# Performance work log

Measured on AMD Instinct MI355X. Metric: run time of the kernel, lower is better.

Reference implementation:

```python
import jax, jax.numpy as jnp
import numpy as np

STATE_DIM, ACTION_DIM, HIDDEN_DIM, GRU_DIM = 256, 64, 1024, 512
BATCH = 65536
IN_DIM = STATE_DIM + ACTION_DIM


def setup_inputs() -> dict:
    key = jax.random.key(0)
    ks = jax.random.split(key, 12)
    s = lambda k, shp, scale: (jax.random.normal(k, shp, jnp.float32) * scale)
    inp = {
        'state': jax.random.normal(ks[0], (BATCH, STATE_DIM), jnp.float32),
        'action': jax.random.normal(ks[1], (BATCH, ACTION_DIM), jnp.float32),
        'hidden': jax.random.normal(ks[2], (1, BATCH, GRU_DIM), jnp.float32),
        # GRU params, PyTorch layout: rows ordered [reset, update, new]
        'w_ih': s(ks[3], (3 * GRU_DIM, IN_DIM), 0.05),
        'w_hh': s(ks[4], (3 * GRU_DIM, GRU_DIM), 0.05),
        'b_ih': jnp.zeros((3 * GRU_DIM,), jnp.float32),
        'b_hh': jnp.zeros((3 * GRU_DIM,), jnp.float32),
        'w1': s(ks[5], (HIDDEN_DIM, GRU_DIM), 0.05),
        'b1': jnp.zeros((HIDDEN_DIM,), jnp.float32),
        'w2': s(ks[6], (HIDDEN_DIM, HIDDEN_DIM), 0.03),
        'b2': jnp.zeros((HIDDEN_DIM,), jnp.float32),
        'w3': s(ks[7], (1, HIDDEN_DIM), 0.03),
        'b3': jnp.zeros((1,), jnp.float32),
    }
    return inp


def reference(state, action, hidden, w_ih, w_hh, b_ih, b_hh, w1, b1, w2, b2, w3, b3):
    # (state, action) -> concat -> single-step GRU -> fc1 -> relu -> fc2 -> relu -> fc3
    sa = jnp.concatenate([state, action], axis=1)          # [B, IN_DIM]
    h = hidden[0]                                           # [B, G]
    gi = sa @ w_ih.T + b_ih                                 # [B, 3G]
    gh = h @ w_hh.T + b_hh                                  # [B, 3G]
    G = h.shape[1]
    i_r, i_z, i_n = gi[:, :G], gi[:, G:2 * G], gi[:, 2 * G:]
    h_r, h_z, h_n = gh[:, :G], gh[:, G:2 * G], gh[:, 2 * G:]
    r = jax.nn.sigmoid(i_r + h_r)
    z = jax.nn.sigmoid(i_z + h_z)
    n = jnp.tanh(i_n + r * h_n)
    h_new = (1.0 - z) * n + z * h                           # [B, G]
    x = jax.nn.relu(h_new @ w1.T + b1)
    x = jax.nn.relu(x @ w2.T + b2)
    q = x @ w3.T + b3                                       # [B, 1]
    return q, h_new[None]
```

## Files before the change

kernel.cpp:

```cpp
#include <hip/hip_runtime.h>
#include <stdint.h>

#define BATCH 65536
#define KCAT 832

typedef __attribute__((ext_vector_type(8))) short bf16x8;
typedef __attribute__((ext_vector_type(4))) float f32x4;

typedef __attribute__((address_space(3))) void lds_void_t;
typedef __attribute__((address_space(1))) void glob_void_t;

__device__ __forceinline__ void async_copy16(const void* g, void* l) {
  __builtin_amdgcn_global_load_lds((glob_void_t*)(uintptr_t)g,
                                   (lds_void_t*)(uint32_t)(uintptr_t)l, 16, 0, 0);
}

__device__ __forceinline__ float b2f(unsigned short u) {
  union { uint32_t i; float f; } c; c.i = ((uint32_t)u) << 16; return c.f;
}
__device__ __forceinline__ unsigned short f2b(float f) {
  uint32_t x = __float_as_uint(f);
  uint32_t r = (x + 0x7fffu + ((x >> 16) & 1u)) >> 16;
  return (unsigned short)r;
}


__global__ void pack_A(const float* __restrict__ state, const float* __restrict__ action,
                       const float* __restrict__ hidden, unsigned short* __restrict__ Acat) {
  long t = (long)blockIdx.x * 256 + threadIdx.x;
  int seg = (int)(t % 104); long row = t / 104;
  int col = seg * 8;
  const float* src;
  if (col < 256)       src = state  + row * 256 + col;
  else if (col < 320)  src = action + row * 64  + (col - 256);
  else                 src = hidden + row * 512 + (col - 320);
  bf16x8 o;
  #pragma unroll
  for (int j = 0; j < 8; j++) o[j] = (short)f2b(src[j]);
  *(bf16x8*)(Acat + row * (size_t)KCAT + col) = o;
}

__global__ void pack_W(const float* __restrict__ w_ih, const float* __restrict__ w_hh,
                       unsigned short* __restrict__ Wrz, unsigned short* __restrict__ Wn) {
  long t = (long)blockIdx.x * 256 + threadIdx.x;
  int seg = (int)(t % 104); int j = (int)(t / 104);
  int col = seg * 8;
  const float* src = (col < 320) ? (w_ih + (long)j * 320 + col)
                                 : (w_hh + (long)j * 512 + (col - 320));
  unsigned short* dst = (j < 1024) ? (Wrz + (long)j * KCAT + col)
                                   : (Wn + (long)(j - 1024) * KCAT + col);
  bf16x8 o;
  #pragma unroll
  for (int jj = 0; jj < 8; jj++) o[jj] = (short)f2b(src[jj]);
  *(bf16x8*)dst = o;
}

__global__ void pack_w12(const float* __restrict__ w1, const float* __restrict__ w2,
                         unsigned short* __restrict__ w1b, unsigned short* __restrict__ w2b) {
  long t = (long)blockIdx.x * 256 + threadIdx.x;
  const float* s; unsigned short* d;
  if (t < 65536) { s = w1 + t * 8; d = w1b + t * 8; }
  else           { long t2 = t - 65536; s = w2 + t2 * 8; d = w2b + t2 * 8; }
  bf16x8 o;
  #pragma unroll
  for (int j = 0; j < 8; j++) o[j] = (short)f2b(s[j]);
  *(bf16x8*)d = o;
}


__global__ __launch_bounds__(256, 2) void gru_fused(
    const unsigned short* __restrict__ A,
    const unsigned short* __restrict__ Wrz,
    const unsigned short* __restrict__ Wn,
    const float* __restrict__ b_ih, const float* __restrict__ b_hh,
    float* __restrict__ hnew_f,
    unsigned short* __restrict__ hnew_b)
{
  __shared__ unsigned short Asm[128 * 64];
  __shared__ unsigned short Wsm[3 * 64 * 64];
  const int tid = threadIdx.x;
  const int wave = tid >> 6, lane = tid & 63;
  const int wm = wave >> 1, wn = wave & 1;

  const int bid = blockIdx.x;
  const int xcd = bid & 7;
  const int j = bid >> 3;
  const int bn = j & 7;
  const long bm = (long)xcd * 64 + (j >> 3);

  const int srow = lane >> 3;
  const int scol = (lane & 7) * 8;

  f32x4 accR[4][2], accZ[4][2], accI[4][2], accH[4][2];
  #pragma unroll
  for (int i = 0; i < 4; i++)
    #pragma unroll
    for (int t = 0; t < 2; t++) {
      accR[i][t] = (f32x4){0.f,0.f,0.f,0.f}; accZ[i][t] = (f32x4){0.f,0.f,0.f,0.f};
      accI[i][t] = (f32x4){0.f,0.f,0.f,0.f}; accH[i][t] = (f32x4){0.f,0.f,0.f,0.f};
    }

  const unsigned short* Ag  = A   + (bm * 128 + wave * 8 + srow) * (size_t)KCAT + scol;
  const unsigned short* Wrg = Wrz + ((size_t)bn * 64 + wave * 8 + srow) * KCAT + scol;
  const unsigned short* Wzg = Wrz + ((size_t)512 + bn * 64 + wave * 8 + srow) * KCAT + scol;
  const unsigned short* Wng = Wn  + ((size_t)bn * 64 + wave * 8 + srow) * KCAT + scol;

  for (int kt = 0; kt < 13; ++kt) {
    __syncthreads();
    #pragma unroll
    for (int t = 0; t < 4; ++t)
      async_copy16(Ag + (size_t)(t * 32) * KCAT + kt * 64, &Asm[(t * 32 + wave * 8) * 64]);
    #pragma unroll
    for (int t = 0; t < 2; ++t) {
      async_copy16(Wrg + (size_t)(t * 32) * KCAT + kt * 64, &Wsm[0 * 4096 + (t * 32 + wave * 8) * 64]);
      async_copy16(Wzg + (size_t)(t * 32) * KCAT + kt * 64, &Wsm[1 * 4096 + (t * 32 + wave * 8) * 64]);
      async_copy16(Wng + (size_t)(t * 32) * KCAT + kt * 64, &Wsm[2 * 4096 + (t * 32 + wave * 8) * 64]);
    }
    __syncthreads();

    #pragma unroll
    for (int ks = 0; ks < 2; ++ks) {
      const int kcol = ks * 32 + (lane >> 4) * 8;
      bf16x8 af[4], bR[2], bZ[2], bN[2];
      #pragma unroll
      for (int mt = 0; mt < 4; mt++)
        af[mt] = *(const bf16x8*)&Asm[(wm * 64 + mt * 16 + (lane & 15)) * 64 + kcol];
      #pragma unroll
      for (int nt = 0; nt < 2; nt++) {
        const int wrow = (wn * 32 + nt * 16 + (lane & 15)) * 64 + kcol;
        bR[nt] = *(const bf16x8*)&Wsm[0 * 4096 + wrow];
        bZ[nt] = *(const bf16x8*)&Wsm[1 * 4096 + wrow];
        bN[nt] = *(const bf16x8*)&Wsm[2 * 4096 + wrow];
      }
      #pragma unroll
      for (int mt = 0; mt < 4; mt++)
        #pragma unroll
        for (int nt = 0; nt < 2; nt++) {
          accR[mt][nt] = __builtin_amdgcn_mfma_f32_16x16x32_bf16(af[mt], bR[nt], accR[mt][nt], 0, 0, 0);
          accZ[mt][nt] = __builtin_amdgcn_mfma_f32_16x16x32_bf16(af[mt], bZ[nt], accZ[mt][nt], 0, 0, 0);
        }
      if (kt < 5) {
        #pragma unroll
        for (int mt = 0; mt < 4; mt++)
          #pragma unroll
          for (int nt = 0; nt < 2; nt++)
            accI[mt][nt] = __builtin_amdgcn_mfma_f32_16x16x32_bf16(af[mt], bN[nt], accI[mt][nt], 0, 0, 0);
      } else {
        #pragma unroll
        for (int mt = 0; mt < 4; mt++)
          #pragma unroll
          for (int nt = 0; nt < 2; nt++)
            accH[mt][nt] = __builtin_amdgcn_mfma_f32_16x16x32_bf16(af[mt], bN[nt], accH[mt][nt], 0, 0, 0);
      }
    }
  }

  const long rowbase = bm * 128 + wm * 64;
  const int colbase = bn * 64 + wn * 32;
  #pragma unroll
  for (int mt = 0; mt < 4; mt++) {
    #pragma unroll
    for (int nt = 0; nt < 2; nt++) {
      const int col = colbase + nt * 16 + (lane & 15);
      const float brv = b_ih[col] + b_hh[col];
      const float bzv = b_ih[512 + col] + b_hh[512 + col];
      const float bin = b_ih[1024 + col];
      const float bhn = b_hh[1024 + col];
      #pragma unroll
      for (int i = 0; i < 4; i++) {
        const long row = rowbase + mt * 16 + (lane >> 4) * 4 + i;
        const float r = 1.f / (1.f + __expf(-(accR[mt][nt][i] + brv)));
        const float z = 1.f / (1.f + __expf(-(accZ[mt][nt][i] + bzv)));
        const float x = (accI[mt][nt][i] + bin) + r * (accH[mt][nt][i] + bhn);
        const float n = 1.f - 2.f / (__expf(2.f * x) + 1.f);
        const float h = b2f(A[row * (size_t)KCAT + 320 + col]);
        const float hv = (1.f - z) * n + z * h;
        hnew_f[row * (size_t)512 + col] = hv;
        hnew_b[row * (size_t)512 + col] = f2b(hv);
      }
    }
  }
}


template<int KT>
__global__ __launch_bounds__(256, 2) void gemm_bt(
    const unsigned short* __restrict__ A, const unsigned short* __restrict__ W,
    const float* __restrict__ bias, unsigned short* __restrict__ out,
    int lda)
{
  __shared__ unsigned short Asm[128 * 64];
  __shared__ unsigned short Bsm[128 * 64];
  const int tid = threadIdx.x;
  const int wave = tid >> 6, lane = tid & 63;
  const int wm = wave >> 1, wn = wave & 1;

  const int bid = blockIdx.x;
  const int xcd = bid & 7;
  const int j = bid >> 3;
  const int bn = j & 7;
  const long bm = (long)xcd * 64 + (j >> 3);

  const int srow = lane >> 3;
  const int scol = (lane & 7) * 8;

  f32x4 acc[4][4];
  #pragma unroll
  for (int i = 0; i < 4; i++)
    #pragma unroll
    for (int t = 0; t < 4; t++) acc[i][t] = (f32x4){0.f, 0.f, 0.f, 0.f};

  const unsigned short* Ag = A + (bm * 128 + wave * 8 + srow) * (size_t)lda + scol;
  const unsigned short* Wg = W + ((size_t)bn * 128 + wave * 8 + srow) * lda + scol;

  for (int kt = 0; kt < KT; ++kt) {
    __syncthreads();
    #pragma unroll
    for (int t = 0; t < 4; ++t)
      async_copy16(Ag + (size_t)(t * 32) * lda + kt * 64, &Asm[(t * 32 + wave * 8) * 64]);
    #pragma unroll
    for (int t = 0; t < 4; ++t)
      async_copy16(Wg + (size_t)(t * 32) * lda + kt * 64, &Bsm[(t * 32 + wave * 8) * 64]);
    __syncthreads();

    #pragma unroll
    for (int ks = 0; ks < 2; ++ks) {
      const int kcol = ks * 32 + (lane >> 4) * 8;
      bf16x8 af[4], bfv[4];
      #pragma unroll
      for (int mt = 0; mt < 4; mt++)
        af[mt] = *(const bf16x8*)&Asm[(wm * 64 + mt * 16 + (lane & 15)) * 64 + kcol];
      #pragma unroll
      for (int nt = 0; nt < 4; nt++)
        bfv[nt] = *(const bf16x8*)&Bsm[(wn * 64 + nt * 16 + (lane & 15)) * 64 + kcol];
      #pragma unroll
      for (int mt = 0; mt < 4; mt++)
        #pragma unroll
        for (int nt = 0; nt < 4; nt++)
          acc[mt][nt] = __builtin_amdgcn_mfma_f32_16x16x32_bf16(af[mt], bfv[nt], acc[mt][nt], 0, 0, 0);
    }
  }

  #pragma unroll
  for (int mt = 0; mt < 4; mt++) {
    #pragma unroll
    for (int nt = 0; nt < 4; nt++) {
      const int col = bn * 128 + wn * 64 + nt * 16 + (lane & 15);
      const float bv = bias[col];
      #pragma unroll
      for (int i = 0; i < 4; i++) {
        const long row = bm * 128 + wm * 64 + mt * 16 + (lane >> 4) * 4 + i;
        float v = fmaxf(acc[mt][nt][i] + bv, 0.f);
        out[row * (size_t)1024 + col] = f2b(v);
      }
    }
  }
}


__global__ void qdot(const unsigned short* __restrict__ x2, const float* __restrict__ w3,
                     const float* __restrict__ b3, float* __restrict__ q) {
  const int lane = threadIdx.x & 63;
  const long row = (long)blockIdx.x * 4 + (threadIdx.x >> 6);
  const unsigned short* xr = x2 + row * (size_t)1024 + lane * 8;
  bf16x8 v0 = *(const bf16x8*)xr;
  bf16x8 v1 = *(const bf16x8*)(xr + 512);
  float s = 0.f;
  #pragma unroll
  for (int j = 0; j < 8; j++) {
    s += b2f((unsigned short)v0[j]) * w3[lane * 8 + j];
    s += b2f((unsigned short)v1[j]) * w3[512 + lane * 8 + j];
  }
  #pragma unroll
  for (int off = 32; off > 0; off >>= 1) s += __shfl_down(s, off, 64);
  if (lane == 0) q[row] = s + b3[0];
}


extern "C" void kernel_launch(void* const* d_in, const int* in_sizes, int n_in,
                              void* d_out, int out_size, void* d_ws, size_t ws_size,
                              hipStream_t stream) {
  const float* state  = (const float*)d_in[0];
  const float* action = (const float*)d_in[1];
  const float* hidden = (const float*)d_in[2];
  const float* w_ih   = (const float*)d_in[3];
  const float* w_hh   = (const float*)d_in[4];
  const float* b_ih   = (const float*)d_in[5];
  const float* b_hh   = (const float*)d_in[6];
  const float* w1     = (const float*)d_in[7];
  const float* b1     = (const float*)d_in[8];
  const float* w2     = (const float*)d_in[9];
  const float* b2     = (const float*)d_in[10];
  const float* w3     = (const float*)d_in[11];
  const float* b3     = (const float*)d_in[12];

  float* q_out = (float*)d_out;
  float* h_out = q_out + BATCH;

  char* ws = (char*)d_ws;
  unsigned short* Acat = (unsigned short*)(ws + 0);
  unsigned short* x1   = (unsigned short*)(ws + 0);
  unsigned short* x2   = (unsigned short*)(ws + 134217728);
  unsigned short* hnb  = (unsigned short*)(ws + 268435456);
  unsigned short* Wrz  = (unsigned short*)(ws + 335544320);
  unsigned short* Wn   = (unsigned short*)(ws + 337248256);
  unsigned short* w1b  = (unsigned short*)(ws + 338100224);
  unsigned short* w2b  = (unsigned short*)(ws + 339148800);

  pack_A<<<26624, 256, 0, stream>>>(state, action, hidden, Acat);
  pack_W<<<624, 256, 0, stream>>>(w_ih, w_hh, Wrz, Wn);
  pack_w12<<<768, 256, 0, stream>>>(w1, w2, w1b, w2b);

  gru_fused<<<4096, 256, 0, stream>>>(Acat, Wrz, Wn, b_ih, b_hh, h_out, hnb);
  gemm_bt<8><<<4096, 256, 0, stream>>>(hnb, w1b, b1, x1, 512);
  gemm_bt<16><<<4096, 256, 0, stream>>>(x1, w2b, b2, x2, 1024);
  qdot<<<16384, 256, 0, stream>>>(x2, w3, b3, q_out);
}
```

Baseline: 821.4 us.

## Swizzle LDS tiles and fuse fc3 dot product into fc2 GEMM epilogue

Applies an XOR swizzle to the LDS column layout in both the GRU and generic GEMM kernels, so MFMA fragment reads avoid bank conflicts. Fuses the final fc3 reduction into the fc2 GEMM epilogue: each block computes partial dot products with w3, reduces them across lanes and atomically adds into q, which is pre-initialized with b3 in the weight pack kernel. This removes the 128MB x2 write/read and the separate qdot launch. In exchange it adds float atomics, whose summation order is nondeterministic.

```diff
diff --git a/kernel.cpp b/kernel.cpp
--- a/kernel.cpp
+++ b/kernel.cpp
@@ -56,15 +56,26 @@
 }
 
 __global__ void pack_w12(const float* __restrict__ w1, const float* __restrict__ w2,
-                         unsigned short* __restrict__ w1b, unsigned short* __restrict__ w2b) {
+                         const float* __restrict__ b3,
+                         unsigned short* __restrict__ w1b, unsigned short* __restrict__ w2b,
+                         float* __restrict__ q) {
   long t = (long)blockIdx.x * 256 + threadIdx.x;
-  const float* s; unsigned short* d;
-  if (t < 65536) { s = w1 + t * 8; d = w1b + t * 8; }
-  else           { long t2 = t - 65536; s = w2 + t2 * 8; d = w2b + t2 * 8; }
-  bf16x8 o;
-  #pragma unroll
-  for (int j = 0; j < 8; j++) o[j] = (short)f2b(s[j]);
-  *(bf16x8*)d = o;
+  if (t < 65536) {
+    const float* s = w1 + t * 8; unsigned short* d = w1b + t * 8;
+    bf16x8 o;
+    #pragma unroll
+    for (int j = 0; j < 8; j++) o[j] = (short)f2b(s[j]);
+    *(bf16x8*)d = o;
+  } else if (t < 196608) {
+    long t2 = t - 65536;
+    const float* s = w2 + t2 * 8; unsigned short* d = w2b + t2 * 8;
+    bf16x8 o;
+    #pragma unroll
+    for (int j = 0; j < 8; j++) o[j] = (short)f2b(s[j]);
+    *(bf16x8*)d = o;
+  } else {
+    q[t - 196608] = b3[0];
+  }
 }
 
 
@@ -89,7 +100,7 @@
   const long bm = (long)xcd * 64 + (j >> 3);
 
   const int srow = lane >> 3;
-  const int scol = (lane & 7) * 8;
+  const int scol = (((lane & 7) ^ srow)) * 8;
 
   f32x4 accR[4][2], accZ[4][2], accI[4][2], accH[4][2];
   #pragma unroll
@@ -105,6 +116,9 @@
   const unsigned short* Wzg = Wrz + ((size_t)512 + bn * 64 + wave * 8 + srow) * KCAT + scol;
   const unsigned short* Wng = Wn  + ((size_t)bn * 64 + wave * 8 + srow) * KCAT + scol;
 
+  const int rlo = lane & 15;
+  const int quad = lane >> 4;
+
   for (int kt = 0; kt < 13; ++kt) {
     __syncthreads();
     #pragma unroll
@@ -120,14 +134,15 @@
 
     #pragma unroll
     for (int ks = 0; ks < 2; ++ks) {
-      const int kcol = ks * 32 + (lane >> 4) * 8;
+      const int kseg = ks * 4 + quad;
+      const int sw = (kseg ^ (rlo & 7)) * 8;
       bf16x8 af[4], bR[2], bZ[2], bN[2];
       #pragma unroll
       for (int mt = 0; mt < 4; mt++)
-        af[mt] = *(const bf16x8*)&Asm[(wm * 64 + mt * 16 + (lane & 15)) * 64 + kcol];
+        af[mt] = *(const bf16x8*)&Asm[(wm * 64 + mt * 16 + rlo) * 64 + sw];
       #pragma unroll
       for (int nt = 0; nt < 2; nt++) {
-        const int wrow = (wn * 32 + nt * 16 + (lane & 15)) * 64 + kcol;
+        const int wrow = (wn * 32 + nt * 16 + rlo) * 64 + sw;
         bR[nt] = *(const bf16x8*)&Wsm[0 * 4096 + wrow];
         bZ[nt] = *(const bf16x8*)&Wsm[1 * 4096 + wrow];
         bN[nt] = *(const bf16x8*)&Wsm[2 * 4096 + wrow];
@@ -161,14 +176,14 @@
   for (int mt = 0; mt < 4; mt++) {
     #pragma unroll
     for (int nt = 0; nt < 2; nt++) {
-      const int col = colbase + nt * 16 + (lane & 15);
+      const int col = colbase + nt * 16 + rlo;
       const float brv = b_ih[col] + b_hh[col];
       const float bzv = b_ih[512 + col] + b_hh[512 + col];
       const float bin = b_ih[1024 + col];
       const float bhn = b_hh[1024 + col];
       #pragma unroll
       for (int i = 0; i < 4; i++) {
-        const long row = rowbase + mt * 16 + (lane >> 4) * 4 + i;
+        const long row = rowbase + mt * 16 + quad * 4 + i;
         const float r = 1.f / (1.f + __expf(-(accR[mt][nt][i] + brv)));
         const float z = 1.f / (1.f + __expf(-(accZ[mt][nt][i] + bzv)));
         const float x = (accI[mt][nt][i] + bin) + r * (accH[mt][nt][i] + bhn);
@@ -183,11 +198,11 @@
 }
 
 
-template<int KT>
+template<int KT, int QFUSE>
 __global__ __launch_bounds__(256, 2) void gemm_bt(
     const unsigned short* __restrict__ A, const unsigned short* __restrict__ W,
     const float* __restrict__ bias, unsigned short* __restrict__ out,
-    int lda)
+    int lda, const float* __restrict__ w3, float* __restrict__ q)
 {
   __shared__ unsigned short Asm[128 * 64];
   __shared__ unsigned short Bsm[128 * 64];
@@ -202,7 +217,7 @@
   const long bm = (long)xcd * 64 + (j >> 3);
 
   const int srow = lane >> 3;
-  const int scol = (lane & 7) * 8;
+  const int scol = (((lane & 7) ^ srow)) * 8;
 
   f32x4 acc[4][4];
   #pragma unroll
@@ -212,6 +227,9 @@
 
   const unsigned short* Ag = A + (bm * 128 + wave * 8 + srow) * (size_t)lda + scol;
   const unsigned short* Wg = W + ((size_t)bn * 128 + wave * 8 + srow) * lda + scol;
+
+  const int rlo = lane & 15;
+  const int quad = lane >> 4;
 
   for (int kt = 0; kt < KT; ++kt) {
     __syncthreads();
@@ -225,14 +243,15 @@
 
     #pragma unroll
     for (int ks = 0; ks < 2; ++ks) {
-      const int kcol = ks * 32 + (lane >> 4) * 8;
+      const int kseg = ks * 4 + quad;
+      const int sw = (kseg ^ (rlo & 7)) * 8;
       bf16x8 af[4], bfv[4];
       #pragma unroll
       for (int mt = 0; mt < 4; mt++)
-        af[mt] = *(const bf16x8*)&Asm[(wm * 64 + mt * 16 + (lane & 15)) * 64 + kcol];
+        af[mt] = *(const bf16x8*)&Asm[(wm * 64 + mt * 16 + rlo) * 64 + sw];
       #pragma unroll
       for (int nt = 0; nt < 4; nt++)
-        bfv[nt] = *(const bf16x8*)&Bsm[(wn * 64 + nt * 16 + (lane & 15)) * 64 + kcol];
+        bfv[nt] = *(const bf16x8*)&Bsm[(wn * 64 + nt * 16 + rlo) * 64 + sw];
       #pragma unroll
       for (int mt = 0; mt < 4; mt++)
         #pragma unroll
@@ -241,39 +260,46 @@
     }
   }
 
-  #pragma unroll
-  for (int mt = 0; mt < 4; mt++) {
+  if (QFUSE == 0) {
+    #pragma unroll
+    for (int mt = 0; mt < 4; mt++) {
+      #pragma unroll
+      for (int nt = 0; nt < 4; nt++) {
+        const int col = bn * 128 + wn * 64 + nt * 16 + rlo;
+        const float bv = bias[col];
+        #pragma unroll
+        for (int i = 0; i < 4; i++) {
+          const long row = bm * 128 + wm * 64 + mt * 16 + quad * 4 + i;
+          float v = fmaxf(acc[mt][nt][i] + bv, 0.f);
+          out[row * (size_t)1024 + col] = f2b(v);
+        }
+      }
+    }
+  } else {
+    float bv[4], w3v[4];
     #pragma unroll
     for (int nt = 0; nt < 4; nt++) {
-      const int col = bn * 128 + wn * 64 + nt * 16 + (lane & 15);
-      const float bv = bias[col];
+      const int col = bn * 128 + wn * 64 + nt * 16 + rlo;
+      bv[nt] = bias[col];
+      w3v[nt] = w3[col];
+    }
+    #pragma unroll
+    for (int mt = 0; mt < 4; mt++) {
       #pragma unroll
       for (int i = 0; i < 4; i++) {
-        const long row = bm * 128 + wm * 64 + mt * 16 + (lane >> 4) * 4 + i;
-        float v = fmaxf(acc[mt][nt][i] + bv, 0.f);
-        out[row * (size_t)1024 + col] = f2b(v);
-      }
-    }
-  }
-}
-
-
-__global__ void qdot(const unsigned short* __restrict__ x2, const float* __restrict__ w3,
-                     const float* __restrict__ b3, float* __restrict__ q) {
-  const int lane = threadIdx.x & 63;
-  const long row = (long)blockIdx.x * 4 + (threadIdx.x >> 6);
-  const unsigned short* xr = x2 + row * (size_t)1024 + lane * 8;
-  bf16x8 v0 = *(const bf16x8*)xr;
-  bf16x8 v1 = *(const bf16x8*)(xr + 512);
-  float s = 0.f;
-  #pragma unroll
-  for (int j = 0; j < 8; j++) {
-    s += b2f((unsigned short)v0[j]) * w3[lane * 8 + j];
-    s += b2f((unsigned short)v1[j]) * w3[512 + lane * 8 + j];
-  }
-  #pragma unroll
-  for (int off = 32; off > 0; off >>= 1) s += __shfl_down(s, off, 64);
-  if (lane == 0) q[row] = s + b3[0];
+        float s = 0.f;
+        #pragma unroll
+        for (int nt = 0; nt < 4; nt++)
+          s += fmaxf(acc[mt][nt][i] + bv[nt], 0.f) * w3v[nt];
+        #pragma unroll
+        for (int off = 1; off < 16; off <<= 1) s += __shfl_xor(s, off, 64);
+        if (rlo == 0) {
+          const long row = bm * 128 + wm * 64 + mt * 16 + quad * 4 + i;
+          atomicAdd(&q[row], s);
+        }
+      }
+    }
+  }
 }
 
 
@@ -300,7 +326,6 @@
   char* ws = (char*)d_ws;
   unsigned short* Acat = (unsigned short*)(ws + 0);
   unsigned short* x1   = (unsigned short*)(ws + 0);
-  unsigned short* x2   = (unsigned short*)(ws + 134217728);
   unsigned short* hnb  = (unsigned short*)(ws + 268435456);
   unsigned short* Wrz  = (unsigned short*)(ws + 335544320);
   unsigned short* Wn   = (unsigned short*)(ws + 337248256);
@@ -309,10 +334,9 @@
 
   pack_A<<<26624, 256, 0, stream>>>(state, action, hidden, Acat);
   pack_W<<<624, 256, 0, stream>>>(w_ih, w_hh, Wrz, Wn);
-  pack_w12<<<768, 256, 0, stream>>>(w1, w2, w1b, w2b);
+  pack_w12<<<1024, 256, 0, stream>>>(w1, w2, b3, w1b, w2b, q_out);
 
   gru_fused<<<4096, 256, 0, stream>>>(Acat, Wrz, Wn, b_ih, b_hh, h_out, hnb);
-  gemm_bt<8><<<4096, 256, 0, stream>>>(hnb, w1b, b1, x1, 512);
-  gemm_bt<16><<<4096, 256, 0, stream>>>(x1, w2b, b2, x2, 1024);
-  qdot<<<16384, 256, 0, stream>>>(x2, w3, b3, q_out);
-}
+  gemm_bt<8, 0><<<4096, 256, 0, stream>>>(hnb, w1b, b1, x1, 512, nullptr, nullptr);
+  gemm_bt<16, 1><<<4096, 256, 0, stream>>>(x1, w2b, b2, nullptr, 1024, w3, q_out);
+}
```

New measurement: 749.8 us. 8.7% less time.
